# Performance work log

Measured on AMD Instinct MI355X. Metric: run time of the kernel, lower is better.

## Reference

```python
import jax, jax.numpy as jnp
import numpy as np

BS, N, HID = 16384, 16, 512  # batch, n coords (state dim = 2n), mlp hidden


def setup_inputs() -> dict:
    key = jax.random.key(0)
    ks = jax.random.split(key, 4)
    d = 2 * N
    x = jax.random.normal(ks[0], (BS, d), dtype=jnp.float32)
    # Lagrangian MLP: 2n -> HID -> HID -> 1 with softplus (smooth 2nd derivs)
    W1 = jax.random.normal(ks[1], (d, HID), dtype=jnp.float32) / np.sqrt(d)
    b1 = jnp.zeros((HID,), jnp.float32)
    W2 = jax.random.normal(ks[2], (HID, HID), dtype=jnp.float32) / np.sqrt(HID)
    b2 = jnp.zeros((HID,), jnp.float32)
    W3 = jax.random.normal(ks[3], (HID, 1), dtype=jnp.float32) / np.sqrt(HID)
    b3 = jnp.zeros((1,), jnp.float32)
    return {"x": x, "W1": W1, "b1": b1, "W2": W2, "b2": b2, "W3": W3, "b3": b3}


def reference(x, W1, b1, W2, b2, W3, b3):
    n = x.shape[1] // 2

    def lagrangian(qqd):  # qqd: [2n] -> scalar
        h = jax.nn.softplus(qqd @ W1 + b1)
        h = jax.nn.softplus(h @ W2 + b2)
        return jnp.sum(h @ W3 + b3)

    # batched first derivative (jacobian of scalar) and hessian; replaces the
    # per-sample python loop of torch.autograd.functional.jacobian/hessian
    jac = jax.vmap(jax.grad(lagrangian))(x)          # [bs, 2n]
    hess = jax.vmap(jax.hessian(lagrangian))(x)      # [bs, 2n, 2n]

    qd = x[:, n:]                                    # [bs, n]
    A = hess[:, n:, n:]                              # d2L/dqd dqd  [bs, n, n]
    B = hess[:, n:, :n]                              # d2L/dqd dq   [bs, n, n]
    rhs = jac[:, :n] - jnp.einsum('bij,bj->bi', B, qd)  # [bs, n]
    qdd = jnp.einsum('bij,bj->bi', jnp.linalg.pinv(A), rhs)  # [bs, n]
    return jnp.concatenate([qd, qdd], axis=1)        # [bs, 2n]
```

## Files before the change

### kernel.cpp

```cpp
#include <hip/hip_runtime.h>
#include <math.h>


#define NSWEEP 5
#define JAX_RCOND 1.9073486e-5

typedef unsigned int uint;
typedef unsigned short ushort;
typedef float f2 __attribute__((ext_vector_type(2)));
typedef float f4 __attribute__((ext_vector_type(4)));
typedef short bf16x8 __attribute__((ext_vector_type(8)));
typedef float f32x16 __attribute__((ext_vector_type(16)));
typedef uint uint2v __attribute__((ext_vector_type(2)));

#define OFF_R    0
#define R_FLOATS 12288
#define OFF_S1   12288
#define OFF_H1   13312
#define OFF_G2   14336
#define OFF_D2   15360
#define OFF_U    16384
#define OFF_X    17408
#define OFF_JAC  17472
#define OFF_T1   17504
#define OFF_T2   18560
#define OFF_AUG  19616
#define SMEM_FLOATS 20160
#define SMEM_BYTES  (SMEM_FLOATS*4)

#define SOLVE_WAVE_DBL 592
#define SOLVE_SMEM_BYTES (4*SOLVE_WAVE_DBL*8)

#define PACK_BYTES 524288

__device__ __forceinline__ ushort f2bf(float x) {
    uint u = __float_as_uint(x);
    return (ushort)((u + 0x7fffu + ((u >> 16) & 1u)) >> 16);
}
__device__ __forceinline__ float bf2f(ushort h) {
    return __uint_as_float(((uint)h) << 16);
}
__device__ __forceinline__ void split3(float x, ushort& h, ushort& m, ushort& l) {
    h = f2bf(x); float r1 = x - bf2f(h);
    m = f2bf(r1); float r2 = r1 - bf2f(m);
    l = f2bf(r2);
}

__device__ __forceinline__ void pairpq(int r, int m, int& p, int& q) {
    p = (m == 0) ? 0 : 1 + (m - 1 + r) % 15;
    q = 1 + (14 - m + r) % 15;
}

__device__ __forceinline__ void wave_fence() {
    __builtin_amdgcn_wave_barrier();
    __builtin_amdgcn_s_waitcnt(0);
    __builtin_amdgcn_wave_barrier();
}

__device__ __forceinline__ void jacobi_solve_wave(
    const float* __restrict__ gaug, double* __restrict__ ws,
    float* __restrict__ outp, int lane)
{
    double* Ad  = ws;
    double* Vd  = Ad + 272;
    double* c8  = Vd + 272;
    double* sn8 = c8 + 8;
    double* il  = sn8 + 8;
    double* yv  = il + 16;

    for (int idx = lane; idx < 272; idx += 64) {
        const int r = idx / 17, c = idx - r*17;
        double a = 0.0;
        if (c < 16) a = 0.5 * ((double)gaug[r*17 + c] + (double)gaug[c*17 + r]);
        Ad[idx] = a;
        Vd[idx] = (c < 16 && r == c) ? 1.0 : 0.0;
    }
    wave_fence();

    for (int sweep = 0; sweep < NSWEEP; ++sweep) {
        for (int rr = 0; rr < 15; ++rr) {
            if (lane < 8) {
                int p, q; pairpq(rr, lane, p, q);
                const double app = Ad[p*17 + p], aqq = Ad[q*17 + q], apq = Ad[p*17 + q];
                double cc = 1.0, ss = 0.0;
                if (apq != 0.0) {
                    const double tau = (aqq - app) / (2.0 * apq);
                    const double tt = ((tau >= 0.0) ? 1.0 : -1.0) / (fabs(tau) + sqrt(1.0 + tau*tau));
                    cc = 1.0 / sqrt(1.0 + tt*tt);
                    ss = tt * cc;
                }
                c8[lane] = cc; sn8[lane] = ss;
            }
            wave_fence();
            #pragma unroll
            for (int k = 0; k < 2; ++k) {
                const int id = lane + 64*k;
                const int m = id >> 4, j = id & 15;
                int p, q; pairpq(rr, m, p, q);
                const double cc = c8[m], ss = sn8[m];
                const double ap = Ad[p*17 + j], aq = Ad[q*17 + j];
                Ad[p*17 + j] = cc*ap - ss*aq;
                Ad[q*17 + j] = ss*ap + cc*aq;
            }
            #pragma unroll
            for (int k = 0; k < 2; ++k) {
                const int id = lane + 64*k;
                const int m = id >> 4, i = id & 15;
                int p, q; pairpq(rr, m, p, q);
                const double cc = c8[m], ss = sn8[m];
                const double vp = Vd[i*17 + p], vq = Vd[i*17 + q];
                Vd[i*17 + p] = cc*vp - ss*vq;
                Vd[i*17 + q] = ss*vp + cc*vq;
            }
            wave_fence();
            #pragma unroll
            for (int k = 0; k < 2; ++k) {
                const int id = lane + 64*k;
                const int m = id >> 4, i = id & 15;
                int p, q; pairpq(rr, m, p, q);
                const double cc = c8[m], ss = sn8[m];
                const double ap = Ad[i*17 + p], aq = Ad[i*17 + q];
                Ad[i*17 + p] = cc*ap - ss*aq;
                Ad[i*17 + q] = ss*ap + cc*aq;
            }
            wave_fence();
        }
    }

    if (lane == 0) {
        double mx = 0.0;
        #pragma unroll
        for (int i = 0; i < 16; ++i) mx = fmax(mx, fabs(Ad[i*17 + i]));
        const double cut = JAX_RCOND * mx;
        #pragma unroll
        for (int i = 0; i < 16; ++i) {
            const double l = Ad[i*17 + i];
            il[i] = (fabs(l) > cut) ? (1.0 / l) : 0.0;
        }
    }
    wave_fence();

    if (lane < 16) {
        double a = 0.0;
        #pragma unroll
        for (int r = 0; r < 16; ++r) a += Vd[r*17 + lane] * (double)gaug[r*17 + 16];
        yv[lane] = a;
    }
    wave_fence();

    if (lane < 16) {
        double a = 0.0;
        #pragma unroll
        for (int i = 0; i < 16; ++i) a += Vd[lane*17 + i] * (il[i] * yv[i]);
        outp[lane] = (float)a;
    }
}

extern "C" __global__ void w1_transpose(const float* __restrict__ W1,
                                        float* __restrict__ W1T) {
    const int t = blockIdx.x * 256 + threadIdx.x;
    W1T[t] = W1[(t & 31) * 512 + (t >> 5)];
}

extern "C" __global__ void w2_pack(const float* __restrict__ W2,
                                   uint* __restrict__ pHi,
                                   uint* __restrict__ pMid,
                                   uint* __restrict__ pLo) {
    const int tid = blockIdx.x * 256 + threadIdx.x;
    const int lane = tid & 63;
    const int k0 = ((tid >> 6) & 31) * 16 + (lane >> 5) * 8;
    const int n  = (tid >> 11) * 32 + (lane & 31);
    uint h[4], m[4], l[4];
    #pragma unroll
    for (int e2 = 0; e2 < 4; ++e2) {
        ushort h0, m0, l0, h1, m1, l1;
        split3(W2[(k0 + 2*e2    )*512 + n], h0, m0, l0);
        split3(W2[(k0 + 2*e2 + 1)*512 + n], h1, m1, l1);
        h[e2] = (uint)h0 | ((uint)h1 << 16);
        m[e2] = (uint)m0 | ((uint)m1 << 16);
        l[e2] = (uint)l0 | ((uint)l1 << 16);
    }
    #pragma unroll
    for (int e2 = 0; e2 < 4; ++e2) {
        pHi [tid*4 + e2] = h[e2];
        pMid[tid*4 + e2] = m[e2];
        pLo [tid*4 + e2] = l[e2];
    }
}

#define MFMA32(A, B, C) __builtin_amdgcn_mfma_f32_32x32x16_bf16((A), (B), (C), 0, 0, 0)

extern "C" __global__ __launch_bounds__(256, 2)
void lnn_kernel(const float* __restrict__ x,
                const float* __restrict__ W1,
                const float* __restrict__ W1T,
                const float* __restrict__ b1,
                const float* __restrict__ W2, const float* __restrict__ b2,
                const float* __restrict__ W3,
                float* __restrict__ out,
                float* __restrict__ aug_g,
                const uint* __restrict__ pHi,
                const uint* __restrict__ pMid,
                const uint* __restrict__ pLo,
                const int solveInMain)
{
    const int b0 = blockIdx.x * 2;
    const int t = threadIdx.x;
    const int lane = t & 63;
    const int w = t >> 6;

    extern __shared__ float sm[];
    char*  A8    = (char*)sm;
    float* s_ws  = sm + OFF_R;
    char*  Mq8   = (char*)sm;
    float* s_s1  = sm + OFF_S1;
    float* s_h1  = sm + OFF_H1;
    float* s_g2  = sm + OFF_G2;
    float* s_d2  = sm + OFF_D2;
    float* s_u   = sm + OFF_U;
    float* s_x   = sm + OFF_X;
    float* s_jac = sm + OFF_JAC;
    float* s_T1  = sm + OFF_T1;
    float* s_T2  = sm + OFF_T2;
    float* s_aug = sm + OFF_AUG;

    if (t < 64) s_x[t] = x[b0*32 + t];
    if (t < 32) {
        const int s = t >> 4, i = t & 15;
        out[(b0+s)*32 + i] = x[(b0+s)*32 + 16 + i];
    }
    __syncthreads();

    #pragma unroll
    for (int rep = 0; rep < 4; ++rep) {
        const int s = rep >> 1;
        const int j = t + (rep & 1)*256;
        float z = b1[j];
        const f4* wt = (const f4*)(W1T + j*32);
        const float* xs = s_x + s*32;
        #pragma unroll
        for (int i4 = 0; i4 < 8; ++i4) {
            const f4 wv = wt[i4];
            z = fmaf(xs[i4*4 + 0], wv.x, z);
            z = fmaf(xs[i4*4 + 1], wv.y, z);
            z = fmaf(xs[i4*4 + 2], wv.z, z);
            z = fmaf(xs[i4*4 + 3], wv.w, z);
        }
        const float e = expf(-fabsf(z));
        const float sg = (z >= 0.f) ? 1.f/(1.f+e) : e/(1.f+e);
        s_s1[s*512 + j] = sg;
        s_h1[s*512 + j] = fmaxf(z, 0.f) + log1pf(e);
    }
    __syncthreads();

    {
        const int c = w*128 + lane*2;
        const f2 bz = *(const f2*)(b2 + c);
        float za[2][2] = { {bz.x, bz.y}, {bz.x, bz.y} };
        #pragma unroll 8
        for (int j = 0; j < 512; ++j) {
            const f2 wv = *(const f2*)(W2 + j*512 + c);
            const float h0 = s_h1[j];
            const float h1 = s_h1[512 + j];
            za[0][0] = fmaf(h0, wv.x, za[0][0]);
            za[0][1] = fmaf(h0, wv.y, za[0][1]);
            za[1][0] = fmaf(h1, wv.x, za[1][0]);
            za[1][1] = fmaf(h1, wv.y, za[1][1]);
        }
        const f2 w3v = *(const f2*)(W3 + c);
        #pragma unroll
        for (int s = 0; s < 2; ++s) {
            const float e0 = expf(-fabsf(za[s][0]));
            const float sg0 = (za[s][0] >= 0.f) ? 1.f/(1.f+e0) : e0/(1.f+e0);
            const float e1v = expf(-fabsf(za[s][1]));
            const float sg1 = (za[s][1] >= 0.f) ? 1.f/(1.f+e1v) : e1v/(1.f+e1v);
            f2 g2v = { w3v.x * sg0, w3v.y * sg1 };
            f2 d2v = { w3v.x * sg0 * (1.f - sg0), w3v.y * sg1 * (1.f - sg1) };
            *(f2*)(s_g2 + s*512 + c) = g2v;
            *(f2*)(s_d2 + s*512 + c) = d2v;
        }
    }
    __syncthreads();

    {
        float g2a[8], g2b[8];
        {
            const float4 ga = *(const float4*)(s_g2 + lane*8);
            const float4 gb = *(const float4*)(s_g2 + lane*8 + 4);
            g2a[0]=ga.x; g2a[1]=ga.y; g2a[2]=ga.z; g2a[3]=ga.w;
            g2a[4]=gb.x; g2a[5]=gb.y; g2a[6]=gb.z; g2a[7]=gb.w;
            const float4 gc = *(const float4*)(s_g2 + 512 + lane*8);
            const float4 gd = *(const float4*)(s_g2 + 512 + lane*8 + 4);
            g2b[0]=gc.x; g2b[1]=gc.y; g2b[2]=gc.z; g2b[3]=gc.w;
            g2b[4]=gd.x; g2b[5]=gd.y; g2b[6]=gd.z; g2b[7]=gd.w;
        }
        for (int jj = 0; jj < 32; ++jj) {
            float pr0[4], pr1[4];
            #pragma unroll
            for (int s4 = 0; s4 < 4; ++s4) {
                const int j = w*128 + jj + s4*32;
                const float4 ra = *(const float4*)(W2 + j*512 + lane*8);
                const float4 rb = *(const float4*)(W2 + j*512 + lane*8 + 4);
                float p0 = ra.x*g2a[0];
                p0 = fmaf(ra.y, g2a[1], p0); p0 = fmaf(ra.z, g2a[2], p0); p0 = fmaf(ra.w, g2a[3], p0);
                p0 = fmaf(rb.x, g2a[4], p0); p0 = fmaf(rb.y, g2a[5], p0);
                p0 = fmaf(rb.z, g2a[6], p0); p0 = fmaf(rb.w, g2a[7], p0);
                pr0[s4] = p0;
                float p1 = ra.x*g2b[0];
                p1 = fmaf(ra.y, g2b[1], p1); p1 = fmaf(ra.z, g2b[2], p1); p1 = fmaf(ra.w, g2b[3], p1);
                p1 = fmaf(rb.x, g2b[4], p1); p1 = fmaf(rb.y, g2b[5], p1);
                p1 = fmaf(rb.z, g2b[6], p1); p1 = fmaf(rb.w, g2b[7], p1);
                pr1[s4] = p1;
            }
            #pragma unroll
            for (int off = 32; off >= 1; off >>= 1) {
                #pragma unroll
                for (int s4 = 0; s4 < 4; ++s4) {
                    pr0[s4] += __shfl_xor(pr0[s4], off);
                    pr1[s4] += __shfl_xor(pr1[s4], off);
                }
            }
            if (lane == 0) {
                #pragma unroll
                for (int s4 = 0; s4 < 4; ++s4) {
                    s_u[w*128 + jj + s4*32]       = pr0[s4];
                    s_u[512 + w*128 + jj + s4*32] = pr1[s4];
                }
            }
        }
    }
    __syncthreads();

    #pragma unroll
    for (int rep = 0; rep < 4; ++rep) {
        const int j = (rep >> 1)*512 + t + (rep & 1)*256;
        const float uj = s_u[j], sv = s_s1[j];
        s_h1[j] = uj * (1.f - sv) / sv;
    }

    const int i5 = 16 + (t >> 4);
    const int c5 = 2 * (t & 15);

    {
        const f4* W1Tv4 = (const f4*)W1T;
        float jacp[2] = {0.f, 0.f};
        float t1a[2] = {0.f, 0.f}, t1b[2] = {0.f, 0.f};

        for (int q = 0; q < 4; ++q) {
            __syncthreads();
            #pragma unroll
            for (int r = 0; r < 4; ++r) {
                const int f = r*256 + t;
                const f4 wv = W1Tv4[q*1024 + f];
                #pragma unroll
                for (int s = 0; s < 2; ++s) {
                    const float sv = s_s1[s*512 + q*128 + (f >> 3)];
                    f4 v = wv;
                    v.x*=sv; v.y*=sv; v.z*=sv; v.w*=sv;
                    ((f4*)(s_ws + s*4096))[f] = v;
                }
            }
            __syncthreads();

            if (w == q) {
                const int i  = t & 15;
                const int jb = (lane >> 4) * 32;
                #pragma unroll
                for (int s = 0; s < 2; ++s) {
                    const float* wsp = s_ws + s*4096;
                    const float* up  = s_u + s*512 + q*128;
                    float jp = jacp[s];
                    #pragma unroll 8
                    for (int jj = 0; jj < 32; ++jj)
                        jp = fmaf(wsp[(jb+jj)*32 + i], up[jb + jj], jp);
                    jacp[s] = jp;
                }
            }

            #pragma unroll
            for (int s = 0; s < 2; ++s) {
                const float* wsp = s_ws + s*4096;
                const float* ep  = s_h1 + s*512 + q*128;
                float a = t1a[s], bv = t1b[s];
                #pragma unroll 4
                for (int jj = 0; jj < 128; ++jj) {
                    const float e   = ep[jj];
                    const float wsi = wsp[jj*32 + i5];
                    const f2 wc = *(const f2*)(wsp + jj*32 + c5);
                    const float tt  = wsi * e;
                    a  = fmaf(tt, wc.x, a);
                    bv = fmaf(tt, wc.y, bv);
                }
                t1a[s] = a; t1b[s] = bv;
            }
        }
        #pragma unroll
        for (int s = 0; s < 2; ++s) {
            s_T1[s*528 + (i5-16)*33 + c5]     = t1a[s];
            s_T1[s*528 + (i5-16)*33 + c5 + 1] = t1b[s];
            s_g2[s*512 + (t>>4)*16 + (t&15)]  = jacp[s];
        }
    }
    __syncthreads();

    if (t < 32) {
        const int s = t >> 4, i = t & 15;
        float p = 0.f;
        #pragma unroll
        for (int seg = 0; seg < 16; ++seg) p += s_g2[s*512 + seg*16 + i];
        s_jac[s*16 + i] = p;
    }

    f32x16 s0n0{}, s0n1{}, s0n2{}, s0n3{};
    f32x16 s1n0{}, s1n1{}, s1n2{}, s1n3{};
    {
        const f4* W1v4 = (const f4*)W1;
        const f4* s1v4 = (const f4*)s_s1;
        const bf16x8* pHiV  = (const bf16x8*)pHi;
        const bf16x8* pMidV = (const bf16x8*)pMid;
        const bf16x8* pLoV  = (const bf16x8*)pLo;
        const int arow = lane & 31;
        const uint abase = (uint)arow * 256u;
        const uint aswz = (uint)(arow & 15);

        #pragma unroll 1
        for (int q = 0; q < 4; ++q) {
            __syncthreads();
            #pragma unroll
            for (int r = 0; r < 4; ++r) {
                const int f = r*256 + t;
                const int i = f >> 5, k4 = f & 31;
                const f4 wv = W1v4[i*128 + q*32 + k4];
                const uint off = (uint)i*256u + (((uint)k4*8u) ^ (((uint)(i & 15)) << 4));
                #pragma unroll
                for (int s = 0; s < 2; ++s) {
                    const f4 sv = s1v4[s*128 + q*32 + k4];
                    ushort h[4], m[4], l[4];
                    split3(wv.x*sv.x, h[0], m[0], l[0]);
                    split3(wv.y*sv.y, h[1], m[1], l[1]);
                    split3(wv.z*sv.z, h[2], m[2], l[2]);
                    split3(wv.w*sv.w, h[3], m[3], l[3]);
                    uint2v vh = { (uint)h[0] | ((uint)h[1]<<16), (uint)h[2] | ((uint)h[3]<<16) };
                    uint2v vm = { (uint)m[0] | ((uint)m[1]<<16), (uint)m[2] | ((uint)m[3]<<16) };
                    uint2v vl = { (uint)l[0] | ((uint)l[1]<<16), (uint)l[2] | ((uint)l[3]<<16) };
                    char* base = A8 + s*24576;
                    *(uint2v*)(base + off)         = vh;
                    *(uint2v*)(base + 8192 + off)  = vm;
                    *(uint2v*)(base + 16384 + off) = vl;
                }
            }
            __syncthreads();

            #pragma unroll 1
            for (int ks8 = 0; ks8 < 8; ++ks8) {
                const uint slot = (uint)(ks8*2 + (lane >> 5));
                const uint aoff = abase + ((slot ^ aswz) << 4);
                const bf16x8 aHi0  = *(const bf16x8*)(A8 + aoff);
                const bf16x8 aMid0 = *(const bf16x8*)(A8 + 8192 + aoff);
                const bf16x8 aLo0  = *(const bf16x8*)(A8 + 16384 + aoff);
                const bf16x8 aHi1  = *(const bf16x8*)(A8 + 24576 + aoff);
                const bf16x8 aMid1 = *(const bf16x8*)(A8 + 24576 + 8192 + aoff);
                const bf16x8 aLo1  = *(const bf16x8*)(A8 + 24576 + 16384 + aoff);
                const int pbase = (w*128 + q*8 + ks8)*64 + lane;
                #define KSTEP(A0, A1, NT) { \
                    const bf16x8 bHi  = pHiV [pbase + (NT)*2048]; \
                    const bf16x8 bMid = pMidV[pbase + (NT)*2048]; \
                    const bf16x8 bLo  = pLoV [pbase + (NT)*2048]; \
                    A0 = MFMA32(aHi0,  bHi,  A0); \
                    A0 = MFMA32(aHi0,  bMid, A0); \
                    A0 = MFMA32(aMid0, bHi,  A0); \
                    A0 = MFMA32(aMid0, bMid, A0); \
                    A0 = MFMA32(aHi0,  bLo,  A0); \
                    A0 = MFMA32(aLo0,  bHi,  A0); \
                    A1 = MFMA32(aHi1,  bHi,  A1); \
                    A1 = MFMA32(aHi1,  bMid, A1); \
                    A1 = MFMA32(aMid1, bHi,  A1); \
                    A1 = MFMA32(aMid1, bMid, A1); \
                    A1 = MFMA32(aHi1,  bLo,  A1); \
                    A1 = MFMA32(aLo1,  bHi,  A1); }
                KSTEP(s0n0, s1n0, 0)
                KSTEP(s0n1, s1n1, 1)
                KSTEP(s0n2, s1n2, 2)
                KSTEP(s0n3, s1n3, 3)
                #undef KSTEP
            }
        }
    }
    __syncthreads();

    {
        float h0acc[2] = {0.f, 0.f}, h1acc[2] = {0.f, 0.f};
        const int rowadd = 4 * (lane >> 5);
        const int cl = lane & 31;
        const uint swi = (uint)((i5 >> 1) & 7);
        const uint swc = (uint)((c5 >> 1) & 7);

        for (int p = 0; p < 4; ++p) {
            if (w == p) {
                #define WRFRAG(ACC, SOFF, NT) { \
                    _Pragma("unroll") \
                    for (int r = 0; r < 16; ++r) { \
                        const int row = (r & 3) + 8*(r >> 2) + rowadd; \
                        const int col = (NT)*32 + cl; \
                        const uint slot = ((uint)(col >> 2)) ^ ((uint)((row >> 1) & 7)); \
                        *(float*)(Mq8 + (SOFF) + row*528 + (slot << 4) + ((col & 3) << 2)) = ACC[r]; \
                    } }
                WRFRAG(s0n0, 0, 0)
                WRFRAG(s0n1, 0, 1)
                WRFRAG(s0n2, 0, 2)
                WRFRAG(s0n3, 0, 3)
                WRFRAG(s1n0, 16896, 0)
                WRFRAG(s1n1, 16896, 1)
                WRFRAG(s1n2, 16896, 2)
                WRFRAG(s1n3, 16896, 3)
                #undef WRFRAG
            }
            __syncthreads();
            #pragma unroll
            for (int s = 0; s < 2; ++s) {
                const f4* d2q = (const f4*)(s_d2 + s*512);
                const char* MiB = Mq8 + s*16896 + i5*528;
                const char* MaB = Mq8 + s*16896 + c5*528;
                const char* MbB = Mq8 + s*16896 + (c5+1)*528;
                float h0 = h0acc[s], h1v = h1acc[s];
                for (int qq = 0; qq < 32; ++qq) {
                    const f4 d  = d2q[p*32 + qq];
                    const f4 mi = *(const f4*)(MiB + (((uint)qq ^ swi) << 4));
                    const f4 ma = *(const f4*)(MaB + (((uint)qq ^ swc) << 4));
                    const f4 mb = *(const f4*)(MbB + (((uint)qq ^ swc) << 4));
                    float tt;
                    tt = mi.x*d.x; h0 = fmaf(tt, ma.x, h0); h1v = fmaf(tt, mb.x, h1v);
                    tt = mi.y*d.y; h0 = fmaf(tt, ma.y, h0); h1v = fmaf(tt, mb.y, h1v);
                    tt = mi.z*d.z; h0 = fmaf(tt, ma.z, h0); h1v = fmaf(tt, mb.z, h1v);
                    tt = mi.w*d.w; h0 = fmaf(tt, ma.w, h0); h1v = fmaf(tt, mb.w, h1v);
                }
                h0acc[s] = h0; h1acc[s] = h1v;
            }
            __syncthreads();
        }
        #pragma unroll
        for (int s = 0; s < 2; ++s) {
            s_T2[s*528 + (i5-16)*33 + c5]     = h0acc[s];
            s_T2[s*528 + (i5-16)*33 + c5 + 1] = h1acc[s];
        }
    }
    __syncthreads();

    {
        const int r = t >> 4, c = t & 15;
        #pragma unroll
        for (int s = 0; s < 2; ++s)
            s_aug[s*272 + r*17 + c] = s_T1[s*528 + r*33 + 16 + c] + s_T2[s*528 + r*33 + 16 + c];
    }
    if (t < 32) {
        const int s = t >> 4, i = t & 15;
        float p = s_jac[s*16 + i];
        #pragma unroll
        for (int c = 0; c < 16; ++c)
            p -= (s_T1[s*528 + i*33 + c] + s_T2[s*528 + i*33 + c]) * s_x[s*32 + 16 + c];
        s_aug[s*272 + i*17 + 16] = p;
    }
    __syncthreads();

    if (!solveInMain) {
        aug_g[b0*272 + t]       = s_aug[t];
        aug_g[b0*272 + 256 + t] = s_aug[256 + t];
        if (t < 32) aug_g[b0*272 + 512 + t] = s_aug[512 + t];
        return;
    }

    if (w >= 2) return;
    jacobi_solve_wave(s_aug + w*272, (double*)sm + w*SOLVE_WAVE_DBL,
                      out + (b0+w)*32 + 16, lane);
}

extern "C" __global__ __launch_bounds__(256, 8)
void lnn_solve(const float* __restrict__ aug_g, float* __restrict__ out)
{
    const int t = threadIdx.x;
    const int lane = t & 63;
    const int w = t >> 6;
    const int b = blockIdx.x * 4 + w;

    extern __shared__ double dsm[];
    jacobi_solve_wave(aug_g + b*272, dsm + w*SOLVE_WAVE_DBL, out + b*32 + 16, lane);
}

extern "C" void kernel_launch(void* const* d_in, const int* in_sizes, int n_in,
                              void* d_out, int out_size, void* d_ws, size_t ws_size,
                              hipStream_t stream) {
    const float* x  = (const float*)d_in[0];
    const float* W1 = (const float*)d_in[1];
    const float* b1 = (const float*)d_in[2];
    const float* W2 = (const float*)d_in[3];
    const float* b2 = (const float*)d_in[4];
    const float* W3 = (const float*)d_in[5];
    float* out = (float*)d_out;

    float* W1T = (float*)d_ws;
    uint*  pHi  = (uint*)((char*)d_ws + 65536);
    uint*  pMid = (uint*)((char*)d_ws + 65536 + PACK_BYTES);
    uint*  pLo  = (uint*)((char*)d_ws + 65536 + 2*PACK_BYTES);
    float* aug  = (float*)((char*)d_ws + 65536 + 3*PACK_BYTES);
    const int bs = in_sizes[0] / 32;

    const size_t need = 65536 + 3*(size_t)PACK_BYTES + (size_t)bs * 272 * 4;
    const int solveInMain = (ws_size < need) ? 1 : 0;

    hipFuncSetAttribute((const void*)lnn_kernel,
                        hipFuncAttributeMaxDynamicSharedMemorySize, SMEM_BYTES);
    w1_transpose<<<dim3(64), dim3(256), 0, stream>>>(W1, W1T);
    w2_pack<<<dim3(128), dim3(256), 0, stream>>>(W2, pHi, pMid, pLo);
    lnn_kernel<<<dim3(bs/2), dim3(256), SMEM_BYTES, stream>>>(
        x, W1, W1T, b1, W2, b2, W3, out, aug, pHi, pMid, pLo, solveInMain);
    if (!solveInMain)
        lnn_solve<<<dim3(bs/4), dim3(256), SOLVE_SMEM_BYTES, stream>>>(aug, out);
}
```

Before: 3.288 ms.

## Alternate phase order across blocks to mix MFMA and VALU work per CU

Moves the kernel phases into inline helper functions and adds a per-block phase order. Blocks whose (blockIdx>>8) bit is set run the MFMA GEMM and the T2 reduction first, then the scalar MLP forward/backward phases; the other blocks keep the original order. The aim is for co-resident blocks on a CU to overlap matrix-core work with VALU and memory-bound work instead of hitting the same bottleneck at the same time. In the GEMM-first order the MFMA accumulators stay live across the scalar phases, and shared buffers are reused in a different order, which raises register pressure and aliasing risk.

```diff
diff --git a/kernel.cpp b/kernel.cpp
--- a/kernel.cpp
+++ b/kernel.cpp
@@ -190,6 +190,304 @@
 
 #define MFMA32(A, B, C) __builtin_amdgcn_mfma_f32_32x32x16_bf16((A), (B), (C), 0, 0, 0)
 
+
+__device__ __forceinline__ void phase_z2(
+    const int lane, const int w,
+    const float* __restrict__ s_h1, float* __restrict__ s_g2, float* __restrict__ s_d2,
+    const float* __restrict__ W2, const float* __restrict__ b2,
+    const float* __restrict__ W3)
+{
+    const int c = w*128 + lane*2;
+    const f2 bz = *(const f2*)(b2 + c);
+    float za[2][2] = { {bz.x, bz.y}, {bz.x, bz.y} };
+    #pragma unroll 8
+    for (int j = 0; j < 512; ++j) {
+        const f2 wv = *(const f2*)(W2 + j*512 + c);
+        const float h0 = s_h1[j];
+        const float h1 = s_h1[512 + j];
+        za[0][0] = fmaf(h0, wv.x, za[0][0]);
+        za[0][1] = fmaf(h0, wv.y, za[0][1]);
+        za[1][0] = fmaf(h1, wv.x, za[1][0]);
+        za[1][1] = fmaf(h1, wv.y, za[1][1]);
+    }
+    const f2 w3v = *(const f2*)(W3 + c);
+    #pragma unroll
+    for (int s = 0; s < 2; ++s) {
+        const float e0 = expf(-fabsf(za[s][0]));
+        const float sg0 = (za[s][0] >= 0.f) ? 1.f/(1.f+e0) : e0/(1.f+e0);
+        const float e1v = expf(-fabsf(za[s][1]));
+        const float sg1 = (za[s][1] >= 0.f) ? 1.f/(1.f+e1v) : e1v/(1.f+e1v);
+        f2 g2v = { w3v.x * sg0, w3v.y * sg1 };
+        f2 d2v = { w3v.x * sg0 * (1.f - sg0), w3v.y * sg1 * (1.f - sg1) };
+        *(f2*)(s_g2 + s*512 + c) = g2v;
+        *(f2*)(s_d2 + s*512 + c) = d2v;
+    }
+}
+
+__device__ __forceinline__ void phase_p3(
+    const int lane, const int w,
+    const float* __restrict__ s_g2, float* __restrict__ s_u,
+    const float* __restrict__ W2)
+{
+    float g2a[8], g2b[8];
+    {
+        const float4 ga = *(const float4*)(s_g2 + lane*8);
+        const float4 gb = *(const float4*)(s_g2 + lane*8 + 4);
+        g2a[0]=ga.x; g2a[1]=ga.y; g2a[2]=ga.z; g2a[3]=ga.w;
+        g2a[4]=gb.x; g2a[5]=gb.y; g2a[6]=gb.z; g2a[7]=gb.w;
+        const float4 gc = *(const float4*)(s_g2 + 512 + lane*8);
+        const float4 gd = *(const float4*)(s_g2 + 512 + lane*8 + 4);
+        g2b[0]=gc.x; g2b[1]=gc.y; g2b[2]=gc.z; g2b[3]=gc.w;
+        g2b[4]=gd.x; g2b[5]=gd.y; g2b[6]=gd.z; g2b[7]=gd.w;
+    }
+    for (int jj = 0; jj < 32; ++jj) {
+        float pr0[4], pr1[4];
+        #pragma unroll
+        for (int s4 = 0; s4 < 4; ++s4) {
+            const int j = w*128 + jj + s4*32;
+            const float4 ra = *(const float4*)(W2 + j*512 + lane*8);
+            const float4 rb = *(const float4*)(W2 + j*512 + lane*8 + 4);
+            float p0 = ra.x*g2a[0];
+            p0 = fmaf(ra.y, g2a[1], p0); p0 = fmaf(ra.z, g2a[2], p0); p0 = fmaf(ra.w, g2a[3], p0);
+            p0 = fmaf(rb.x, g2a[4], p0); p0 = fmaf(rb.y, g2a[5], p0);
+            p0 = fmaf(rb.z, g2a[6], p0); p0 = fmaf(rb.w, g2a[7], p0);
+            pr0[s4] = p0;
+            float p1 = ra.x*g2b[0];
+            p1 = fmaf(ra.y, g2b[1], p1); p1 = fmaf(ra.z, g2b[2], p1); p1 = fmaf(ra.w, g2b[3], p1);
+            p1 = fmaf(rb.x, g2b[4], p1); p1 = fmaf(rb.y, g2b[5], p1);
+            p1 = fmaf(rb.z, g2b[6], p1); p1 = fmaf(rb.w, g2b[7], p1);
+            pr1[s4] = p1;
+        }
+        #pragma unroll
+        for (int off = 32; off >= 1; off >>= 1) {
+            #pragma unroll
+            for (int s4 = 0; s4 < 4; ++s4) {
+                pr0[s4] += __shfl_xor(pr0[s4], off);
+                pr1[s4] += __shfl_xor(pr1[s4], off);
+            }
+        }
+        if (lane == 0) {
+            #pragma unroll
+            for (int s4 = 0; s4 < 4; ++s4) {
+                s_u[w*128 + jj + s4*32]       = pr0[s4];
+                s_u[512 + w*128 + jj + s4*32] = pr1[s4];
+            }
+        }
+    }
+}
+
+__device__ __forceinline__ void phase_p45(
+    const int t, const int lane, const int w, const int i5, const int c5,
+    const float* __restrict__ W1T, const float* __restrict__ s_s1,
+    const float* __restrict__ s_h1, const float* __restrict__ s_u,
+    float* __restrict__ s_ws, float* __restrict__ s_T1, float* __restrict__ s_g2)
+{
+    const f4* W1Tv4 = (const f4*)W1T;
+    float jacp[2] = {0.f, 0.f};
+    float t1a[2] = {0.f, 0.f}, t1b[2] = {0.f, 0.f};
+
+    for (int q = 0; q < 4; ++q) {
+        __syncthreads();
+        #pragma unroll
+        for (int r = 0; r < 4; ++r) {
+            const int f = r*256 + t;
+            const f4 wv = W1Tv4[q*1024 + f];
+            #pragma unroll
+            for (int s = 0; s < 2; ++s) {
+                const float sv = s_s1[s*512 + q*128 + (f >> 3)];
+                f4 v = wv;
+                v.x*=sv; v.y*=sv; v.z*=sv; v.w*=sv;
+                ((f4*)(s_ws + s*4096))[f] = v;
+            }
+        }
+        __syncthreads();
+
+        if (w == q) {
+            const int i  = t & 15;
+            const int jb = (lane >> 4) * 32;
+            #pragma unroll
+            for (int s = 0; s < 2; ++s) {
+                const float* wsp = s_ws + s*4096;
+                const float* up  = s_u + s*512 + q*128;
+                float jp = jacp[s];
+                #pragma unroll 8
+                for (int jj = 0; jj < 32; ++jj)
+                    jp = fmaf(wsp[(jb+jj)*32 + i], up[jb + jj], jp);
+                jacp[s] = jp;
+            }
+        }
+
+        #pragma unroll
+        for (int s = 0; s < 2; ++s) {
+            const float* wsp = s_ws + s*4096;
+            const float* ep  = s_h1 + s*512 + q*128;
+            float a = t1a[s], bv = t1b[s];
+            #pragma unroll 4
+            for (int jj = 0; jj < 128; ++jj) {
+                const float e   = ep[jj];
+                const float wsi = wsp[jj*32 + i5];
+                const f2 wc = *(const f2*)(wsp + jj*32 + c5);
+                const float tt  = wsi * e;
+                a  = fmaf(tt, wc.x, a);
+                bv = fmaf(tt, wc.y, bv);
+            }
+            t1a[s] = a; t1b[s] = bv;
+        }
+    }
+    #pragma unroll
+    for (int s = 0; s < 2; ++s) {
+        s_T1[s*528 + (i5-16)*33 + c5]     = t1a[s];
+        s_T1[s*528 + (i5-16)*33 + c5 + 1] = t1b[s];
+        s_g2[s*512 + (t>>4)*16 + (t&15)]  = jacp[s];
+    }
+    __syncthreads();
+}
+
+__device__ __forceinline__ void run_gemm(
+    const int t, const int lane, const int w,
+    char* __restrict__ A8, const float* __restrict__ s_s1,
+    const float* __restrict__ W1,
+    const uint* __restrict__ pHi, const uint* __restrict__ pMid,
+    const uint* __restrict__ pLo,
+    f32x16& s0n0, f32x16& s0n1, f32x16& s0n2, f32x16& s0n3,
+    f32x16& s1n0, f32x16& s1n1, f32x16& s1n2, f32x16& s1n3)
+{
+    const f4* W1v4 = (const f4*)W1;
+    const f4* s1v4 = (const f4*)s_s1;
+    const bf16x8* pHiV  = (const bf16x8*)pHi;
+    const bf16x8* pMidV = (const bf16x8*)pMid;
+    const bf16x8* pLoV  = (const bf16x8*)pLo;
+    const int arow = lane & 31;
+    const uint abase = (uint)arow * 256u;
+    const uint aswz = (uint)(arow & 15);
+
+    #pragma unroll 1
+    for (int q = 0; q < 4; ++q) {
+        __syncthreads();
+        #pragma unroll
+        for (int r = 0; r < 4; ++r) {
+            const int f = r*256 + t;
+            const int i = f >> 5, k4 = f & 31;
+            const f4 wv = W1v4[i*128 + q*32 + k4];
+            const uint off = (uint)i*256u + (((uint)k4*8u) ^ (((uint)(i & 15)) << 4));
+            #pragma unroll
+            for (int s = 0; s < 2; ++s) {
+                const f4 sv = s1v4[s*128 + q*32 + k4];
+                ushort h[4], m[4], l[4];
+                split3(wv.x*sv.x, h[0], m[0], l[0]);
+                split3(wv.y*sv.y, h[1], m[1], l[1]);
+                split3(wv.z*sv.z, h[2], m[2], l[2]);
+                split3(wv.w*sv.w, h[3], m[3], l[3]);
+                uint2v vh = { (uint)h[0] | ((uint)h[1]<<16), (uint)h[2] | ((uint)h[3]<<16) };
+                uint2v vm = { (uint)m[0] | ((uint)m[1]<<16), (uint)m[2] | ((uint)m[3]<<16) };
+                uint2v vl = { (uint)l[0] | ((uint)l[1]<<16), (uint)l[2] | ((uint)l[3]<<16) };
+                char* base = A8 + s*24576;
+                *(uint2v*)(base + off)         = vh;
+                *(uint2v*)(base + 8192 + off)  = vm;
+                *(uint2v*)(base + 16384 + off) = vl;
+            }
+        }
+        __syncthreads();
+
+        #pragma unroll 1
+        for (int ks8 = 0; ks8 < 8; ++ks8) {
+            const uint slot = (uint)(ks8*2 + (lane >> 5));
+            const uint aoff = abase + ((slot ^ aswz) << 4);
+            const bf16x8 aHi0  = *(const bf16x8*)(A8 + aoff);
+            const bf16x8 aMid0 = *(const bf16x8*)(A8 + 8192 + aoff);
+            const bf16x8 aLo0  = *(const bf16x8*)(A8 + 16384 + aoff);
+            const bf16x8 aHi1  = *(const bf16x8*)(A8 + 24576 + aoff);
+            const bf16x8 aMid1 = *(const bf16x8*)(A8 + 24576 + 8192 + aoff);
+            const bf16x8 aLo1  = *(const bf16x8*)(A8 + 24576 + 16384 + aoff);
+            const int pbase = (w*128 + q*8 + ks8)*64 + lane;
+            #define KSTEP(A0, A1, NT) { \
+                const bf16x8 bHi  = pHiV [pbase + (NT)*2048]; \
+                const bf16x8 bMid = pMidV[pbase + (NT)*2048]; \
+                const bf16x8 bLo  = pLoV [pbase + (NT)*2048]; \
+                A0 = MFMA32(aHi0,  bHi,  A0); \
+                A0 = MFMA32(aHi0,  bMid, A0); \
+                A0 = MFMA32(aMid0, bHi,  A0); \
+                A0 = MFMA32(aMid0, bMid, A0); \
+                A0 = MFMA32(aHi0,  bLo,  A0); \
+                A0 = MFMA32(aLo0,  bHi,  A0); \
+                A1 = MFMA32(aHi1,  bHi,  A1); \
+                A1 = MFMA32(aHi1,  bMid, A1); \
+                A1 = MFMA32(aMid1, bHi,  A1); \
+                A1 = MFMA32(aMid1, bMid, A1); \
+                A1 = MFMA32(aHi1,  bLo,  A1); \
+                A1 = MFMA32(aLo1,  bHi,  A1); }
+            KSTEP(s0n0, s1n0, 0)
+            KSTEP(s0n1, s1n1, 1)
+            KSTEP(s0n2, s1n2, 2)
+            KSTEP(s0n3, s1n3, 3)
+            #undef KSTEP
+        }
+    }
+}
+
+__device__ __forceinline__ void run_p7(
+    const int lane, const int w, const int i5, const int c5,
+    char* __restrict__ Mq8, const float* __restrict__ s_d2,
+    float* __restrict__ s_T2,
+    const f32x16& s0n0, const f32x16& s0n1, const f32x16& s0n2, const f32x16& s0n3,
+    const f32x16& s1n0, const f32x16& s1n1, const f32x16& s1n2, const f32x16& s1n3)
+{
+    float h0acc[2] = {0.f, 0.f}, h1acc[2] = {0.f, 0.f};
+    const int rowadd = 4 * (lane >> 5);
+    const int cl = lane & 31;
+    const uint swi = (uint)((i5 >> 1) & 7);
+    const uint swc = (uint)((c5 >> 1) & 7);
+
+    for (int p = 0; p < 4; ++p) {
+        if (w == p) {
+            #define WRFRAG(ACC, SOFF, NT) { \
+                _Pragma("unroll") \
+                for (int r = 0; r < 16; ++r) { \
+                    const int row = (r & 3) + 8*(r >> 2) + rowadd; \
+                    const int col = (NT)*32 + cl; \
+                    const uint slot = ((uint)(col >> 2)) ^ ((uint)((row >> 1) & 7)); \
+                    *(float*)(Mq8 + (SOFF) + row*528 + (slot << 4) + ((col & 3) << 2)) = ACC[r]; \
+                } }
+            WRFRAG(s0n0, 0, 0)
+            WRFRAG(s0n1, 0, 1)
+            WRFRAG(s0n2, 0, 2)
+            WRFRAG(s0n3, 0, 3)
+            WRFRAG(s1n0, 16896, 0)
+            WRFRAG(s1n1, 16896, 1)
+            WRFRAG(s1n2, 16896, 2)
+            WRFRAG(s1n3, 16896, 3)
+            #undef WRFRAG
+        }
+        __syncthreads();
+        #pragma unroll
+        for (int s = 0; s < 2; ++s) {
+            const f4* d2q = (const f4*)(s_d2 + s*512);
+            const char* MiB = Mq8 + s*16896 + i5*528;
+            const char* MaB = Mq8 + s*16896 + c5*528;
+            const char* MbB = Mq8 + s*16896 + (c5+1)*528;
+            float h0 = h0acc[s], h1v = h1acc[s];
+            for (int qq = 0; qq < 32; ++qq) {
+                const f4 d  = d2q[p*32 + qq];
+                const f4 mi = *(const f4*)(MiB + (((uint)qq ^ swi) << 4));
+                const f4 ma = *(const f4*)(MaB + (((uint)qq ^ swc) << 4));
+                const f4 mb = *(const f4*)(MbB + (((uint)qq ^ swc) << 4));
+                float tt;
+                tt = mi.x*d.x; h0 = fmaf(tt, ma.x, h0); h1v = fmaf(tt, mb.x, h1v);
+                tt = mi.y*d.y; h0 = fmaf(tt, ma.y, h0); h1v = fmaf(tt, mb.y, h1v);
+                tt = mi.z*d.z; h0 = fmaf(tt, ma.z, h0); h1v = fmaf(tt, mb.z, h1v);
+                tt = mi.w*d.w; h0 = fmaf(tt, ma.w, h0); h1v = fmaf(tt, mb.w, h1v);
+            }
+            h0acc[s] = h0; h1acc[s] = h1v;
+        }
+        __syncthreads();
+    }
+    #pragma unroll
+    for (int s = 0; s < 2; ++s) {
+        s_T2[s*528 + (i5-16)*33 + c5]     = h0acc[s];
+        s_T2[s*528 + (i5-16)*33 + c5 + 1] = h1acc[s];
+    }
+}
+
 extern "C" __global__ __launch_bounds__(256, 2)
 void lnn_kernel(const float* __restrict__ x,
                 const float* __restrict__ W1,
@@ -253,298 +551,67 @@
     }
     __syncthreads();
 
-    {
-        const int c = w*128 + lane*2;
-        const f2 bz = *(const f2*)(b2 + c);
-        float za[2][2] = { {bz.x, bz.y}, {bz.x, bz.y} };
-        #pragma unroll 8
-        for (int j = 0; j < 512; ++j) {
-            const f2 wv = *(const f2*)(W2 + j*512 + c);
-            const float h0 = s_h1[j];
-            const float h1 = s_h1[512 + j];
-            za[0][0] = fmaf(h0, wv.x, za[0][0]);
-            za[0][1] = fmaf(h0, wv.y, za[0][1]);
-            za[1][0] = fmaf(h1, wv.x, za[1][0]);
-            za[1][1] = fmaf(h1, wv.y, za[1][1]);
-        }
-        const f2 w3v = *(const f2*)(W3 + c);
-        #pragma unroll
-        for (int s = 0; s < 2; ++s) {
-            const float e0 = expf(-fabsf(za[s][0]));
-            const float sg0 = (za[s][0] >= 0.f) ? 1.f/(1.f+e0) : e0/(1.f+e0);
-            const float e1v = expf(-fabsf(za[s][1]));
-            const float sg1 = (za[s][1] >= 0.f) ? 1.f/(1.f+e1v) : e1v/(1.f+e1v);
-            f2 g2v = { w3v.x * sg0, w3v.y * sg1 };
-            f2 d2v = { w3v.x * sg0 * (1.f - sg0), w3v.y * sg1 * (1.f - sg1) };
-            *(f2*)(s_g2 + s*512 + c) = g2v;
-            *(f2*)(s_d2 + s*512 + c) = d2v;
-        }
-    }
-    __syncthreads();
-
-    {
-        float g2a[8], g2b[8];
-        {
-            const float4 ga = *(const float4*)(s_g2 + lane*8);
-            const float4 gb = *(const float4*)(s_g2 + lane*8 + 4);
-            g2a[0]=ga.x; g2a[1]=ga.y; g2a[2]=ga.z; g2a[3]=ga.w;
-            g2a[4]=gb.x; g2a[5]=gb.y; g2a[6]=gb.z; g2a[7]=gb.w;
-            const float4 gc = *(const float4*)(s_g2 + 512 + lane*8);
-            const float4 gd = *(const float4*)(s_g2 + 512 + lane*8 + 4);
-            g2b[0]=gc.x; g2b[1]=gc.y; g2b[2]=gc.z; g2b[3]=gc.w;
-            g2b[4]=gd.x; g2b[5]=gd.y; g2b[6]=gd.z; g2b[7]=gd.w;
-        }
-        for (int jj = 0; jj < 32; ++jj) {
-            float pr0[4], pr1[4];
-            #pragma unroll
-            for (int s4 = 0; s4 < 4; ++s4) {
-                const int j = w*128 + jj + s4*32;
-                const float4 ra = *(const float4*)(W2 + j*512 + lane*8);
-                const float4 rb = *(const float4*)(W2 + j*512 + lane*8 + 4);
-                float p0 = ra.x*g2a[0];
-                p0 = fmaf(ra.y, g2a[1], p0); p0 = fmaf(ra.z, g2a[2], p0); p0 = fmaf(ra.w, g2a[3], p0);
-                p0 = fmaf(rb.x, g2a[4], p0); p0 = fmaf(rb.y, g2a[5], p0);
-                p0 = fmaf(rb.z, g2a[6], p0); p0 = fmaf(rb.w, g2a[7], p0);
-                pr0[s4] = p0;
-                float p1 = ra.x*g2b[0];
-                p1 = fmaf(ra.y, g2b[1], p1); p1 = fmaf(ra.z, g2b[2], p1); p1 = fmaf(ra.w, g2b[3], p1);
-                p1 = fmaf(rb.x, g2b[4], p1); p1 = fmaf(rb.y, g2b[5], p1);
-                p1 = fmaf(rb.z, g2b[6], p1); p1 = fmaf(rb.w, g2b[7], p1);
-                pr1[s4] = p1;
-            }
-            #pragma unroll
-            for (int off = 32; off >= 1; off >>= 1) {
-                #pragma unroll
-                for (int s4 = 0; s4 < 4; ++s4) {
-                    pr0[s4] += __shfl_xor(pr0[s4], off);
-                    pr1[s4] += __shfl_xor(pr1[s4], off);
-                }
-            }
-            if (lane == 0) {
-                #pragma unroll
-                for (int s4 = 0; s4 < 4; ++s4) {
-                    s_u[w*128 + jj + s4*32]       = pr0[s4];
-                    s_u[512 + w*128 + jj + s4*32] = pr1[s4];
-                }
-            }
-        }
-    }
-    __syncthreads();
-
-    #pragma unroll
-    for (int rep = 0; rep < 4; ++rep) {
-        const int j = (rep >> 1)*512 + t + (rep & 1)*256;
-        const float uj = s_u[j], sv = s_s1[j];
-        s_h1[j] = uj * (1.f - sv) / sv;
-    }
-
     const int i5 = 16 + (t >> 4);
     const int c5 = 2 * (t & 15);
 
-    {
-        const f4* W1Tv4 = (const f4*)W1T;
-        float jacp[2] = {0.f, 0.f};
-        float t1a[2] = {0.f, 0.f}, t1b[2] = {0.f, 0.f};
-
-        for (int q = 0; q < 4; ++q) {
-            __syncthreads();
-            #pragma unroll
-            for (int r = 0; r < 4; ++r) {
-                const int f = r*256 + t;
-                const f4 wv = W1Tv4[q*1024 + f];
-                #pragma unroll
-                for (int s = 0; s < 2; ++s) {
-                    const float sv = s_s1[s*512 + q*128 + (f >> 3)];
-                    f4 v = wv;
-                    v.x*=sv; v.y*=sv; v.z*=sv; v.w*=sv;
-                    ((f4*)(s_ws + s*4096))[f] = v;
-                }
-            }
-            __syncthreads();
-
-            if (w == q) {
-                const int i  = t & 15;
-                const int jb = (lane >> 4) * 32;
-                #pragma unroll
-                for (int s = 0; s < 2; ++s) {
-                    const float* wsp = s_ws + s*4096;
-                    const float* up  = s_u + s*512 + q*128;
-                    float jp = jacp[s];
-                    #pragma unroll 8
-                    for (int jj = 0; jj < 32; ++jj)
-                        jp = fmaf(wsp[(jb+jj)*32 + i], up[jb + jj], jp);
-                    jacp[s] = jp;
-                }
-            }
-
-            #pragma unroll
-            for (int s = 0; s < 2; ++s) {
-                const float* wsp = s_ws + s*4096;
-                const float* ep  = s_h1 + s*512 + q*128;
-                float a = t1a[s], bv = t1b[s];
-                #pragma unroll 4
-                for (int jj = 0; jj < 128; ++jj) {
-                    const float e   = ep[jj];
-                    const float wsi = wsp[jj*32 + i5];
-                    const f2 wc = *(const f2*)(wsp + jj*32 + c5);
-                    const float tt  = wsi * e;
-                    a  = fmaf(tt, wc.x, a);
-                    bv = fmaf(tt, wc.y, bv);
-                }
-                t1a[s] = a; t1b[s] = bv;
-            }
-        }
-        #pragma unroll
-        for (int s = 0; s < 2; ++s) {
-            s_T1[s*528 + (i5-16)*33 + c5]     = t1a[s];
-            s_T1[s*528 + (i5-16)*33 + c5 + 1] = t1b[s];
-            s_g2[s*512 + (t>>4)*16 + (t&15)]  = jacp[s];
-        }
-    }
-    __syncthreads();
-
-    if (t < 32) {
-        const int s = t >> 4, i = t & 15;
-        float p = 0.f;
-        #pragma unroll
-        for (int seg = 0; seg < 16; ++seg) p += s_g2[s*512 + seg*16 + i];
-        s_jac[s*16 + i] = p;
-    }
-
-    f32x16 s0n0{}, s0n1{}, s0n2{}, s0n3{};
-    f32x16 s1n0{}, s1n1{}, s1n2{}, s1n3{};
-    {
-        const f4* W1v4 = (const f4*)W1;
-        const f4* s1v4 = (const f4*)s_s1;
-        const bf16x8* pHiV  = (const bf16x8*)pHi;
-        const bf16x8* pMidV = (const bf16x8*)pMid;
-        const bf16x8* pLoV  = (const bf16x8*)pLo;
-        const int arow = lane & 31;
-        const uint abase = (uint)arow * 256u;
-        const uint aswz = (uint)(arow & 15);
-
-        #pragma unroll 1
-        for (int q = 0; q < 4; ++q) {
-            __syncthreads();
-            #pragma unroll
-            for (int r = 0; r < 4; ++r) {
-                const int f = r*256 + t;
-                const int i = f >> 5, k4 = f & 31;
-                const f4 wv = W1v4[i*128 + q*32 + k4];
-                const uint off = (uint)i*256u + (((uint)k4*8u) ^ (((uint)(i & 15)) << 4));
-                #pragma unroll
-                for (int s = 0; s < 2; ++s) {
-                    const f4 sv = s1v4[s*128 + q*32 + k4];
-                    ushort h[4], m[4], l[4];
-                    split3(wv.x*sv.x, h[0], m[0], l[0]);
-                    split3(wv.y*sv.y, h[1], m[1], l[1]);
-                    split3(wv.z*sv.z, h[2], m[2], l[2]);
-                    split3(wv.w*sv.w, h[3], m[3], l[3]);
-                    uint2v vh = { (uint)h[0] | ((uint)h[1]<<16), (uint)h[2] | ((uint)h[3]<<16) };
-                    uint2v vm = { (uint)m[0] | ((uint)m[1]<<16), (uint)m[2] | ((uint)m[3]<<16) };
-                    uint2v vl = { (uint)l[0] | ((uint)l[1]<<16), (uint)l[2] | ((uint)l[3]<<16) };
-                    char* base = A8 + s*24576;
-                    *(uint2v*)(base + off)         = vh;
-                    *(uint2v*)(base + 8192 + off)  = vm;
-                    *(uint2v*)(base + 16384 + off) = vl;
-                }
-            }
-            __syncthreads();
-
-            #pragma unroll 1
-            for (int ks8 = 0; ks8 < 8; ++ks8) {
-                const uint slot = (uint)(ks8*2 + (lane >> 5));
-                const uint aoff = abase + ((slot ^ aswz) << 4);
-                const bf16x8 aHi0  = *(const bf16x8*)(A8 + aoff);
-                const bf16x8 aMid0 = *(const bf16x8*)(A8 + 8192 + aoff);
-                const bf16x8 aLo0  = *(const bf16x8*)(A8 + 16384 + aoff);
-                const bf16x8 aHi1  = *(const bf16x8*)(A8 + 24576 + aoff);
-                const bf16x8 aMid1 = *(const bf16x8*)(A8 + 24576 + 8192 + aoff);
-                const bf16x8 aLo1  = *(const bf16x8*)(A8 + 24576 + 16384 + aoff);
-                const int pbase = (w*128 + q*8 + ks8)*64 + lane;
-                #define KSTEP(A0, A1, NT) { \
-                    const bf16x8 bHi  = pHiV [pbase + (NT)*2048]; \
-                    const bf16x8 bMid = pMidV[pbase + (NT)*2048]; \
-                    const bf16x8 bLo  = pLoV [pbase + (NT)*2048]; \
-                    A0 = MFMA32(aHi0,  bHi,  A0); \
-                    A0 = MFMA32(aHi0,  bMid, A0); \
-                    A0 = MFMA32(aMid0, bHi,  A0); \
-                    A0 = MFMA32(aMid0, bMid, A0); \
-                    A0 = MFMA32(aHi0,  bLo,  A0); \
-                    A0 = MFMA32(aLo0,  bHi,  A0); \
-                    A1 = MFMA32(aHi1,  bHi,  A1); \
-                    A1 = MFMA32(aHi1,  bMid, A1); \
-                    A1 = MFMA32(aMid1, bHi,  A1); \
-                    A1 = MFMA32(aMid1, bMid, A1); \
-                    A1 = MFMA32(aHi1,  bLo,  A1); \
-                    A1 = MFMA32(aLo1,  bHi,  A1); }
-                KSTEP(s0n0, s1n0, 0)
-                KSTEP(s0n1, s1n1, 1)
-                KSTEP(s0n2, s1n2, 2)
-                KSTEP(s0n3, s1n3, 3)
-                #undef KSTEP
-            }
-        }
-    }
-    __syncthreads();
-
-    {
-        float h0acc[2] = {0.f, 0.f}, h1acc[2] = {0.f, 0.f};
-        const int rowadd = 4 * (lane >> 5);
-        const int cl = lane & 31;
-        const uint swi = (uint)((i5 >> 1) & 7);
-        const uint swc = (uint)((c5 >> 1) & 7);
-
-        for (int p = 0; p < 4; ++p) {
-            if (w == p) {
-                #define WRFRAG(ACC, SOFF, NT) { \
-                    _Pragma("unroll") \
-                    for (int r = 0; r < 16; ++r) { \
-                        const int row = (r & 3) + 8*(r >> 2) + rowadd; \
-                        const int col = (NT)*32 + cl; \
-                        const uint slot = ((uint)(col >> 2)) ^ ((uint)((row >> 1) & 7)); \
-                        *(float*)(Mq8 + (SOFF) + row*528 + (slot << 4) + ((col & 3) << 2)) = ACC[r]; \
-                    } }
-                WRFRAG(s0n0, 0, 0)
-                WRFRAG(s0n1, 0, 1)
-                WRFRAG(s0n2, 0, 2)
-                WRFRAG(s0n3, 0, 3)
-                WRFRAG(s1n0, 16896, 0)
-                WRFRAG(s1n1, 16896, 1)
-                WRFRAG(s1n2, 16896, 2)
-                WRFRAG(s1n3, 16896, 3)
-                #undef WRFRAG
-            }
-            __syncthreads();
-            #pragma unroll
-            for (int s = 0; s < 2; ++s) {
-                const f4* d2q = (const f4*)(s_d2 + s*512);
-                const char* MiB = Mq8 + s*16896 + i5*528;
-                const char* MaB = Mq8 + s*16896 + c5*528;
-                const char* MbB = Mq8 + s*16896 + (c5+1)*528;
-                float h0 = h0acc[s], h1v = h1acc[s];
-                for (int qq = 0; qq < 32; ++qq) {
-                    const f4 d  = d2q[p*32 + qq];
-                    const f4 mi = *(const f4*)(MiB + (((uint)qq ^ swi) << 4));
-                    const f4 ma = *(const f4*)(MaB + (((uint)qq ^ swc) << 4));
-                    const f4 mb = *(const f4*)(MbB + (((uint)qq ^ swc) << 4));
-                    float tt;
-                    tt = mi.x*d.x; h0 = fmaf(tt, ma.x, h0); h1v = fmaf(tt, mb.x, h1v);
-                    tt = mi.y*d.y; h0 = fmaf(tt, ma.y, h0); h1v = fmaf(tt, mb.y, h1v);
-                    tt = mi.z*d.z; h0 = fmaf(tt, ma.z, h0); h1v = fmaf(tt, mb.z, h1v);
-                    tt = mi.w*d.w; h0 = fmaf(tt, ma.w, h0); h1v = fmaf(tt, mb.w, h1v);
-                }
-                h0acc[s] = h0; h1acc[s] = h1v;
-            }
-            __syncthreads();
-        }
-        #pragma unroll
-        for (int s = 0; s < 2; ++s) {
-            s_T2[s*528 + (i5-16)*33 + c5]     = h0acc[s];
-            s_T2[s*528 + (i5-16)*33 + c5 + 1] = h1acc[s];
-        }
-    }
-    __syncthreads();
+    const bool gemmFirst = ((blockIdx.x >> 8) & 1) != 0;
+
+    if (gemmFirst) {
+        f32x16 s0n0{}, s0n1{}, s0n2{}, s0n3{};
+        f32x16 s1n0{}, s1n1{}, s1n2{}, s1n3{};
+        run_gemm(t, lane, w, A8, s_s1, W1, pHi, pMid, pLo,
+                 s0n0, s0n1, s0n2, s0n3, s1n0, s1n1, s1n2, s1n3);
+        __syncthreads();
+        phase_z2(lane, w, s_h1, s_g2, s_d2, W2, b2, W3);
+        __syncthreads();
+        run_p7(lane, w, i5, c5, Mq8, s_d2, s_T2,
+               s0n0, s0n1, s0n2, s0n3, s1n0, s1n1, s1n2, s1n3);
+        __syncthreads();
+        phase_p3(lane, w, s_g2, s_u, W2);
+        __syncthreads();
+        #pragma unroll
+        for (int rep = 0; rep < 4; ++rep) {
+            const int j = (rep >> 1)*512 + t + (rep & 1)*256;
+            const float uj = s_u[j], sv = s_s1[j];
+            s_h1[j] = uj * (1.f - sv) / sv;
+        }
+        phase_p45(t, lane, w, i5, c5, W1T, s_s1, s_h1, s_u, s_ws, s_T1, s_g2);
+        if (t < 32) {
+            const int s = t >> 4, i = t & 15;
+            float p = 0.f;
+            #pragma unroll
+            for (int seg = 0; seg < 16; ++seg) p += s_g2[s*512 + seg*16 + i];
+            s_jac[s*16 + i] = p;
+        }
+        __syncthreads();
+    } else {
+        phase_z2(lane, w, s_h1, s_g2, s_d2, W2, b2, W3);
+        __syncthreads();
+        phase_p3(lane, w, s_g2, s_u, W2);
+        __syncthreads();
+        #pragma unroll
+        for (int rep = 0; rep < 4; ++rep) {
+            const int j = (rep >> 1)*512 + t + (rep & 1)*256;
+            const float uj = s_u[j], sv = s_s1[j];
+            s_h1[j] = uj * (1.f - sv) / sv;
+        }
+        phase_p45(t, lane, w, i5, c5, W1T, s_s1, s_h1, s_u, s_ws, s_T1, s_g2);
+        if (t < 32) {
+            const int s = t >> 4, i = t & 15;
+            float p = 0.f;
+            #pragma unroll
+            for (int seg = 0; seg < 16; ++seg) p += s_g2[s*512 + seg*16 + i];
+            s_jac[s*16 + i] = p;
+        }
+        f32x16 s0n0{}, s0n1{}, s0n2{}, s0n3{};
+        f32x16 s1n0{}, s1n1{}, s1n2{}, s1n3{};
+        run_gemm(t, lane, w, A8, s_s1, W1, pHi, pMid, pLo,
+                 s0n0, s0n1, s0n2, s0n3, s1n0, s1n1, s1n2, s1n3);
+        __syncthreads();
+        run_p7(lane, w, i5, c5, Mq8, s_d2, s_T2,
+               s0n0, s0n1, s0n2, s0n3, s1n0, s1n1, s1n2, s1n3);
+        __syncthreads();
+    }
 
     {
         const int r = t >> 4, c = t & 15;
```

Measured after the change: 3.426 ms. 1.04x slower.
